# Optimization experiments

Measured on AMD Instinct MI355X. Metric: run time of the kernel, lower is better.

The kernel has to match this reference:

```python
import jax, jax.numpy as jnp
import numpy as np

H = 512          # hidden_size
B, S, L = 32, 2048, 2
D = 2 * H        # encoder output / hidden feature dim


def setup_inputs() -> dict:
    key = jax.random.key(0)
    ks = jax.random.split(key, 9)
    lim1 = 1.0 / np.sqrt(D)
    limv = 1.0 / np.sqrt(H)
    return {
        "hidden": jax.random.normal(ks[0], (L, B, D), jnp.float32),
        "encoder_outputs": jax.random.normal(ks[1], (B, S, D), jnp.float32),
        "mask": jax.random.randint(ks[2], (B, S), 0, 2, jnp.int32),
        "W1_w": jax.random.uniform(ks[3], (H, D), jnp.float32, -lim1, lim1),
        "W1_b": jax.random.uniform(ks[4], (H,), jnp.float32, -lim1, lim1),
        "W2_w": jax.random.uniform(ks[5], (H, D), jnp.float32, -lim1, lim1),
        "W2_b": jax.random.uniform(ks[6], (H,), jnp.float32, -lim1, lim1),
        "V_w": jax.random.uniform(ks[7], (1, H), jnp.float32, -limv, limv),
        "V_b": jax.random.uniform(ks[8], (1,), jnp.float32, -limv, limv),
    }


def reference(hidden, encoder_outputs, mask, W1_w, W1_b, W2_w, W2_b, V_w, V_b):
    # query: last layer hidden state, broadcast over sequence -> [B, 1, D]
    query = hidden[-1][:, None, :]
    # W1(enc) + W2(query): [B, S, H]
    proj = (jnp.einsum('bsd,hd->bsh', encoder_outputs, W1_w) + W1_b
            + jnp.einsum('bqd,hd->bqh', query, W2_w) + W2_b)
    # V projection -> scores [B, S]
    score = jnp.einsum('bsh,h->bs', jnp.tanh(proj), V_w[0]) + V_b[0]
    score = jnp.where(mask == 0, jnp.float32(-1e9), score)
    attn_weights = jax.nn.softmax(score, axis=1)          # [B, S]
    context = jnp.einsum('bs,bsd->bd', attn_weights, encoder_outputs)  # [B, D]
    return context, attn_weights
```

## Files before the change

### kernel.cpp

```cpp
#include <hip/hip_runtime.h>
#include <hip/hip_bf16.h>

#define B_ 32
#define S_ 2048
#define D_ 1024
#define H_ 512
#define M_ (B_*S_)
#define BM 128
#define BN 128
#define BK 64
#define TILE (BM*BK)

typedef __attribute__((ext_vector_type(8))) short short8;
typedef __attribute__((ext_vector_type(4))) float f32x4;

__device__ __forceinline__ unsigned short f2bf(float f){
  return __builtin_bit_cast(unsigned short, __float2bfloat16(f));
}

__device__ __forceinline__ float fast_tanh(float x){
  return 1.f - 2.f*__builtin_amdgcn_rcpf(__expf(2.f*x) + 1.f);
}

__device__ __forceinline__ int swz(int row, int kshort){
  return row*BK + ((kshort & 56) ^ ((row&7)<<3)) + (kshort & 7);
}

__global__ __launch_bounds__(256) void convw_kernel(
    const float* __restrict__ W1, unsigned short* __restrict__ W1s){
  int tid = blockIdx.x*256 + threadIdx.x;
  int n = tid*8;
  int h = n >> 10;
  int k = n & 1023;
  int bn = h >> 7, row = h & 127;
  int kt = k >> 6, kk = k & 63;
  float4 lo = *(const float4*)(W1 + n);
  float4 hi = *(const float4*)(W1 + n + 4);
  short8 r;
  r[0]=(short)f2bf(lo.x); r[1]=(short)f2bf(lo.y); r[2]=(short)f2bf(lo.z); r[3]=(short)f2bf(lo.w);
  r[4]=(short)f2bf(hi.x); r[5]=(short)f2bf(hi.y); r[6]=(short)f2bf(hi.z); r[7]=(short)f2bf(hi.w);
  *(short8*)&W1s[(bn*16 + kt)*TILE + swz(row, kk)] = r;
}

__global__ __launch_bounds__(256) void qbias_kernel(
    const float* __restrict__ hidden, const float* __restrict__ W2,
    const float* __restrict__ W1b, const float* __restrict__ W2b,
    float* __restrict__ qb){
  int b = blockIdx.x, h0 = blockIdx.y*64;
  int wave = threadIdx.x>>6, lane = threadIdx.x&63;
  const float* q = hidden + (size_t)(B_ + b)*D_;
  for (int i=0;i<16;i++){
    int h = h0 + wave*16 + i;
    const float* w = W2 + (size_t)h*D_;
    float s = 0.f;
    #pragma unroll
    for (int it=0; it<4; ++it){
      int d = it*256 + lane*4;
      const float4 qq = *(const float4*)(q+d);
      const float4 ww = *(const float4*)(w+d);
      s += qq.x*ww.x + qq.y*ww.y + qq.z*ww.z + qq.w*ww.w;
    }
    #pragma unroll
    for (int off=1; off<64; off<<=1) s += __shfl_xor(s, off);
    if (lane==0) qb[b*H_ + h] = s + W1b[h] + W2b[h];
  }
}

__global__ __launch_bounds__(256, 3) void score_gemm(
    const float* __restrict__ enc, const unsigned short* __restrict__ W1s,
    const float* __restrict__ qb, const float* __restrict__ Vw,
    float* __restrict__ score_p){
  const int id  = blockIdx.x;
  const int xcd = id & 7;
  const int j   = id >> 3;
  const int bm  = xcd*64 + (j >> 2);
  const int bn  = j & 3;
  const int m0 = bm*BM, h0 = bn*BN;
  const int tid = threadIdx.x, lane = tid&63, wave = tid>>6;
  const int wm = (wave>>1)*64, wn = (wave&1)*64;

  __shared__ __align__(16) unsigned short As[TILE];
  __shared__ __align__(16) unsigned short Bs[2][TILE];

  f32x4 acc[4][4];
  #pragma unroll
  for (int i=0;i<4;i++)
    #pragma unroll
    for (int j2=0;j2<4;j2++)
      acc[i][j2] = (f32x4)(0.f);

  float4 aLo[4], aHi[4];

#define LOAD_A(KT) do{ const int kkx=(KT)*BK; \
  _Pragma("unroll") for (int i=0;i<4;i++){ \
    int c=tid+i*256; int row=c>>3, kc=(c&7)*8; \
    const float4* pa=(const float4*)(enc+(size_t)(m0+row)*D_+kkx+kc); \
    aLo[i]=pa[0]; aHi[i]=pa[1]; } }while(0)

#define GLD_B(KT,P) do{ const unsigned short* bsrc=W1s+(size_t)(bn*16+(KT))*TILE; \
  _Pragma("unroll") for (int i=0;i<4;i++){ \
    __builtin_amdgcn_global_load_lds( \
      (const __attribute__((address_space(1))) unsigned int*)(bsrc+i*2048+tid*8), \
      (__attribute__((address_space(3))) unsigned int*)&Bs[P][i*2048+tid*8], 16,0,0); } }while(0)

#define CVT_A() do{ \
  _Pragma("unroll") for (int i=0;i<4;i++){ \
    int c=tid+i*256; int row=c>>3, kc=(c&7)*8; short8 av; \
    av[0]=(short)f2bf(aLo[i].x); av[1]=(short)f2bf(aLo[i].y); \
    av[2]=(short)f2bf(aLo[i].z); av[3]=(short)f2bf(aLo[i].w); \
    av[4]=(short)f2bf(aHi[i].x); av[5]=(short)f2bf(aHi[i].y); \
    av[6]=(short)f2bf(aHi[i].z); av[7]=(short)f2bf(aHi[i].w); \
    *(short8*)&As[swz(row,kc)] = av; } }while(0)

#define COMPUTE(P) do{ \
  _Pragma("unroll") for (int kh=0; kh<2; ++kh){ \
    const int kb = kh*32 + (lane>>4)*8; \
    short8 af[4], bf[4]; \
    _Pragma("unroll") for (int mi=0;mi<4;mi++){ \
      int row=wm+mi*16+(lane&15); af[mi]=*(const short8*)&As[swz(row,kb)]; } \
    _Pragma("unroll") for (int ni=0;ni<4;ni++){ \
      int row=wn+ni*16+(lane&15); bf[ni]=*(const short8*)&Bs[P][swz(row,kb)]; } \
    _Pragma("unroll") for (int mi=0;mi<4;mi++) \
      _Pragma("unroll") for (int ni=0;ni<4;ni++) \
        acc[mi][ni]=__builtin_amdgcn_mfma_f32_16x16x32_bf16(af[mi],bf[ni],acc[mi][ni],0,0,0); \
  } }while(0)

  LOAD_A(0);
  GLD_B(0,0);
  CVT_A();
  LOAD_A(1);
  GLD_B(1,1);
  asm volatile("s_waitcnt vmcnt(12) lgkmcnt(0)" ::: "memory");
  __builtin_amdgcn_s_barrier();

  #pragma unroll 2
  for (int kt=0; kt<14; ++kt){
    const int p = kt&1;
    COMPUTE(p);
    __builtin_amdgcn_s_barrier();
    GLD_B(kt+2, p);
    CVT_A();
    LOAD_A(kt+2);
    asm volatile("s_waitcnt lgkmcnt(0)" ::: "memory");
    __builtin_amdgcn_s_barrier();
  }
  COMPUTE(0);
  __builtin_amdgcn_s_barrier();
  CVT_A();
  asm volatile("s_waitcnt lgkmcnt(0)" ::: "memory");
  __builtin_amdgcn_s_barrier();
  COMPUTE(1);

  const int bidx = m0 >> 11;
  float qv[4], vwv[4];
  #pragma unroll
  for (int ni=0;ni<4;ni++){
    int h = h0 + wn + ni*16 + (lane&15);
    qv[ni]  = qb[bidx*H_ + h];
    vwv[ni] = Vw[h];
  }
  __shared__ float psum[4][BM];
  #pragma unroll
  for (int mi=0;mi<4;mi++){
    #pragma unroll
    for (int r=0;r<4;r++){
      float s = 0.f;
      #pragma unroll
      for (int ni=0;ni<4;ni++) s += fast_tanh(acc[mi][ni][r] + qv[ni]) * vwv[ni];
      s += __shfl_xor(s,1); s += __shfl_xor(s,2);
      s += __shfl_xor(s,4); s += __shfl_xor(s,8);
      if ((lane&15)==0){
        int m = wm + mi*16 + ((lane>>4)<<2) + r;
        psum[wave][m] = s;
      }
    }
  }
  __syncthreads();
  if (tid < BM){
    int w0 = (tid>>6)*2;
    score_p[(size_t)bn*M_ + m0 + tid] = psum[w0][tid] + psum[w0+1][tid];
  }
}

__global__ __launch_bounds__(256) void softmax_kernel(
    const float* __restrict__ score_p, const int* __restrict__ mask,
    float* __restrict__ attn){
  int b = blockIdx.x, tid = threadIdx.x;
  int wave = tid>>6, lane = tid&63;
  __shared__ float red[8];
  float v[8];
  float mx = -1e30f;
  #pragma unroll
  for (int i=0;i<8;i++){
    int idx = b*S_ + tid + i*256;
    float sc = score_p[idx] + score_p[M_+idx] + score_p[2*M_+idx] + score_p[3*M_+idx];
    v[i] = (mask[idx]==0) ? -1e9f : sc;
    mx = fmaxf(mx, v[i]);
  }
  #pragma unroll
  for (int off=1; off<64; off<<=1) mx = fmaxf(mx, __shfl_xor(mx, off));
  if (lane==0) red[wave] = mx;
  __syncthreads();
  mx = fmaxf(fmaxf(red[0],red[1]), fmaxf(red[2],red[3]));
  float sum = 0.f;
  #pragma unroll
  for (int i=0;i<8;i++){ v[i] = __expf(v[i]-mx); sum += v[i]; }
  #pragma unroll
  for (int off=1; off<64; off<<=1) sum += __shfl_xor(sum, off);
  if (lane==0) red[4+wave] = sum;
  __syncthreads();
  float inv = 1.f/(red[4]+red[5]+red[6]+red[7]);
  #pragma unroll
  for (int i=0;i<8;i++) attn[b*S_ + tid + i*256] = v[i]*inv;
}

__global__ __launch_bounds__(256) void context_kernel(
    const float* __restrict__ enc, const float* __restrict__ attn,
    float* __restrict__ ctx){
  int b = blockIdx.x, sc = blockIdx.y;
  int s0 = sc*64;
  int d4 = threadIdx.x*4;
  const float* ep = enc + ((size_t)b*S_ + s0)*D_ + d4;
  const float* ap = attn + b*S_ + s0;
  float4 a0 = make_float4(0.f,0.f,0.f,0.f);
  float4 a1 = make_float4(0.f,0.f,0.f,0.f);
  #pragma unroll 4
  for (int i=0;i<64;i+=2){
    float w0 = ap[i], w1 = ap[i+1];
    float4 e0 = *(const float4*)(ep + (size_t)i*D_);
    float4 e1 = *(const float4*)(ep + (size_t)(i+1)*D_);
    a0.x = fmaf(w0, e0.x, a0.x); a0.y = fmaf(w0, e0.y, a0.y);
    a0.z = fmaf(w0, e0.z, a0.z); a0.w = fmaf(w0, e0.w, a0.w);
    a1.x = fmaf(w1, e1.x, a1.x); a1.y = fmaf(w1, e1.y, a1.y);
    a1.z = fmaf(w1, e1.z, a1.z); a1.w = fmaf(w1, e1.w, a1.w);
  }
  float* o = ctx + b*D_ + d4;
  atomicAdd(o+0, a0.x+a1.x); atomicAdd(o+1, a0.y+a1.y);
  atomicAdd(o+2, a0.z+a1.z); atomicAdd(o+3, a0.w+a1.w);
}

extern "C" void kernel_launch(void* const* d_in, const int* in_sizes, int n_in,
                              void* d_out, int out_size, void* d_ws, size_t ws_size,
                              hipStream_t stream){
  const float* hidden = (const float*)d_in[0];
  const float* enc    = (const float*)d_in[1];
  const int*   mask   = (const int*)d_in[2];
  const float* W1w    = (const float*)d_in[3];
  const float* W1b    = (const float*)d_in[4];
  const float* W2w    = (const float*)d_in[5];
  const float* W2b    = (const float*)d_in[6];
  const float* Vw     = (const float*)d_in[7];
  float* out = (float*)d_out;

  float* qb           = (float*)d_ws;
  float* score_p      = qb + B_*H_;
  unsigned short* W1s = (unsigned short*)(score_p + 4*M_);

  hipMemsetAsync(out, 0, (size_t)B_*D_*sizeof(float), stream);

  convw_kernel  <<<H_*D_/8/256,     256, 0, stream>>>(W1w, W1s);
  qbias_kernel  <<<dim3(B_, H_/64), 256, 0, stream>>>(hidden, W2w, W1b, W2b, qb);
  score_gemm    <<<4*(M_/BM),       256, 0, stream>>>(enc, W1s, qb, Vw, score_p);
  softmax_kernel<<<B_,              256, 0, stream>>>(score_p, mask, out + B_*D_);
  context_kernel<<<dim3(B_, 32),    256, 0, stream>>>(enc, out + B_*D_, out);
}
```

Measured before the change: 187.3 us.

## Load W1 fragments directly into registers in MFMA order, double-buffer A in LDS

The weight conversion kernel now writes W1 in a per-lane MFMA fragment order, so the GEMM can load B operands straight from global memory into registers (register double-buffered) instead of staging them through LDS. LDS is repurposed as a double buffer for the converted A tile, which removes one barrier per k-step. The cost is higher register pressure (occupancy hint lowered from 3 to 2) and B being fetched per wave from global/L2 rather than shared across the block.

```diff
diff --git a/kernel.cpp b/kernel.cpp
--- a/kernel.cpp
+++ b/kernel.cpp
@@ -27,19 +27,19 @@
 }
 
 __global__ __launch_bounds__(256) void convw_kernel(
-    const float* __restrict__ W1, unsigned short* __restrict__ W1s){
-  int tid = blockIdx.x*256 + threadIdx.x;
-  int n = tid*8;
-  int h = n >> 10;
-  int k = n & 1023;
-  int bn = h >> 7, row = h & 127;
-  int kt = k >> 6, kk = k & 63;
-  float4 lo = *(const float4*)(W1 + n);
-  float4 hi = *(const float4*)(W1 + n + 4);
-  short8 r;
-  r[0]=(short)f2bf(lo.x); r[1]=(short)f2bf(lo.y); r[2]=(short)f2bf(lo.z); r[3]=(short)f2bf(lo.w);
-  r[4]=(short)f2bf(hi.x); r[5]=(short)f2bf(hi.y); r[6]=(short)f2bf(hi.z); r[7]=(short)f2bf(hi.w);
-  *(short8*)&W1s[(bn*16 + kt)*TILE + swz(row, kk)] = r;
+    const float* __restrict__ W1, unsigned short* __restrict__ W1f){
+  int g = blockIdx.x*256 + threadIdx.x;
+  int lane = g & 63, r = g >> 6;
+  int kh = r & 1, ni = (r>>1)&3, wh = (r>>3)&1, kt = (r>>4)&15, bn = r>>8;
+  int h  = bn*128 + wh*64 + ni*16 + (lane&15);
+  int k0 = kt*64 + kh*32 + (lane>>4)*8;
+  const float* src = W1 + (size_t)h*D_ + k0;
+  float4 lo = *(const float4*)src;
+  float4 hi = *(const float4*)(src+4);
+  short8 v;
+  v[0]=(short)f2bf(lo.x); v[1]=(short)f2bf(lo.y); v[2]=(short)f2bf(lo.z); v[3]=(short)f2bf(lo.w);
+  v[4]=(short)f2bf(hi.x); v[5]=(short)f2bf(hi.y); v[6]=(short)f2bf(hi.z); v[7]=(short)f2bf(hi.w);
+  *(short8*)&W1f[(size_t)g*8] = v;
 }
 
 __global__ __launch_bounds__(256) void qbias_kernel(
@@ -66,8 +66,8 @@
   }
 }
 
-__global__ __launch_bounds__(256, 3) void score_gemm(
-    const float* __restrict__ enc, const unsigned short* __restrict__ W1s,
+__global__ __launch_bounds__(256, 2) void score_gemm(
+    const float* __restrict__ enc, const unsigned short* __restrict__ W1f,
     const float* __restrict__ qb, const float* __restrict__ Vw,
     float* __restrict__ score_p){
   const int id  = blockIdx.x;
@@ -77,10 +77,9 @@
   const int bn  = j & 3;
   const int m0 = bm*BM, h0 = bn*BN;
   const int tid = threadIdx.x, lane = tid&63, wave = tid>>6;
-  const int wm = (wave>>1)*64, wn = (wave&1)*64;
-
-  __shared__ __align__(16) unsigned short As[TILE];
-  __shared__ __align__(16) unsigned short Bs[2][TILE];
+  const int wm = (wave>>1)*64, wh = wave&1, wn = wh*64;
+
+  __shared__ __align__(16) unsigned short As[2][TILE];
 
   f32x4 acc[4][4];
   #pragma unroll
@@ -90,6 +89,7 @@
       acc[i][j2] = (f32x4)(0.f);
 
   float4 aLo[4], aHi[4];
+  short8 b0[4][2], b1[4][2];
 
 #define LOAD_A(KT) do{ const int kkx=(KT)*BK; \
   _Pragma("unroll") for (int i=0;i<4;i++){ \
@@ -97,59 +97,59 @@
     const float4* pa=(const float4*)(enc+(size_t)(m0+row)*D_+kkx+kc); \
     aLo[i]=pa[0]; aHi[i]=pa[1]; } }while(0)
 
-#define GLD_B(KT,P) do{ const unsigned short* bsrc=W1s+(size_t)(bn*16+(KT))*TILE; \
-  _Pragma("unroll") for (int i=0;i<4;i++){ \
-    __builtin_amdgcn_global_load_lds( \
-      (const __attribute__((address_space(1))) unsigned int*)(bsrc+i*2048+tid*8), \
-      (__attribute__((address_space(3))) unsigned int*)&Bs[P][i*2048+tid*8], 16,0,0); } }while(0)
-
-#define CVT_A() do{ \
+#define CVT_A(P) do{ \
   _Pragma("unroll") for (int i=0;i<4;i++){ \
     int c=tid+i*256; int row=c>>3, kc=(c&7)*8; short8 av; \
     av[0]=(short)f2bf(aLo[i].x); av[1]=(short)f2bf(aLo[i].y); \
     av[2]=(short)f2bf(aLo[i].z); av[3]=(short)f2bf(aLo[i].w); \
     av[4]=(short)f2bf(aHi[i].x); av[5]=(short)f2bf(aHi[i].y); \
     av[6]=(short)f2bf(aHi[i].z); av[7]=(short)f2bf(aHi[i].w); \
-    *(short8*)&As[swz(row,kc)] = av; } }while(0)
-
-#define COMPUTE(P) do{ \
+    *(short8*)&As[P][swz(row,kc)] = av; } }while(0)
+
+#define GLOB_B(KT, BB) do{ \
+  const size_t sb = (size_t)(((bn*16+(KT))*2+wh)*8)*512 + lane*8; \
+  _Pragma("unroll") for (int ni=0;ni<4;ni++) \
+    _Pragma("unroll") for (int kh=0;kh<2;kh++) \
+      BB[ni][kh] = *(const short8*)&W1f[sb + (size_t)(ni*2+kh)*512]; }while(0)
+
+#define COMPUTE(P, BB) do{ \
   _Pragma("unroll") for (int kh=0; kh<2; ++kh){ \
     const int kb = kh*32 + (lane>>4)*8; \
-    short8 af[4], bf[4]; \
+    short8 af[4]; \
     _Pragma("unroll") for (int mi=0;mi<4;mi++){ \
-      int row=wm+mi*16+(lane&15); af[mi]=*(const short8*)&As[swz(row,kb)]; } \
-    _Pragma("unroll") for (int ni=0;ni<4;ni++){ \
-      int row=wn+ni*16+(lane&15); bf[ni]=*(const short8*)&Bs[P][swz(row,kb)]; } \
+      int row=wm+mi*16+(lane&15); af[mi]=*(const short8*)&As[P][swz(row,kb)]; } \
     _Pragma("unroll") for (int mi=0;mi<4;mi++) \
       _Pragma("unroll") for (int ni=0;ni<4;ni++) \
-        acc[mi][ni]=__builtin_amdgcn_mfma_f32_16x16x32_bf16(af[mi],bf[ni],acc[mi][ni],0,0,0); \
+        acc[mi][ni]=__builtin_amdgcn_mfma_f32_16x16x32_bf16(af[mi],BB[ni][kh],acc[mi][ni],0,0,0); \
   } }while(0)
 
+#define BODY(KT, BC, BN_) do{ \
+  GLOB_B((KT)+1, BN_); \
+  __builtin_amdgcn_sched_barrier(0); \
+  COMPUTE((KT)&1, BC); \
+  CVT_A(((KT)+1)&1); \
+  LOAD_A((KT)+2); \
+  asm volatile("s_waitcnt lgkmcnt(0)" ::: "memory"); \
+  __builtin_amdgcn_s_barrier(); }while(0)
+
   LOAD_A(0);
-  GLD_B(0,0);
-  CVT_A();
+  GLOB_B(0, b0);
+  CVT_A(0);
   LOAD_A(1);
-  GLD_B(1,1);
-  asm volatile("s_waitcnt vmcnt(12) lgkmcnt(0)" ::: "memory");
-  __builtin_amdgcn_s_barrier();
-
-  #pragma unroll 2
-  for (int kt=0; kt<14; ++kt){
-    const int p = kt&1;
-    COMPUTE(p);
-    __builtin_amdgcn_s_barrier();
-    GLD_B(kt+2, p);
-    CVT_A();
-    LOAD_A(kt+2);
-    asm volatile("s_waitcnt lgkmcnt(0)" ::: "memory");
-    __builtin_amdgcn_s_barrier();
-  }
-  COMPUTE(0);
-  __builtin_amdgcn_s_barrier();
-  CVT_A();
   asm volatile("s_waitcnt lgkmcnt(0)" ::: "memory");
   __builtin_amdgcn_s_barrier();
-  COMPUTE(1);
+
+  for (int k2=0; k2<7; ++k2){
+    BODY(2*k2,   b0, b1);
+    BODY(2*k2+1, b1, b0);
+  }
+  GLOB_B(15, b1);
+  __builtin_amdgcn_sched_barrier(0);
+  COMPUTE(0, b0);
+  CVT_A(1);
+  asm volatile("s_waitcnt lgkmcnt(0)" ::: "memory");
+  __builtin_amdgcn_s_barrier();
+  COMPUTE(1, b1);
 
   const int bidx = m0 >> 11;
   float qv[4], vwv[4];
@@ -254,13 +254,13 @@
 
   float* qb           = (float*)d_ws;
   float* score_p      = qb + B_*H_;
-  unsigned short* W1s = (unsigned short*)(score_p + 4*M_);
+  unsigned short* W1f = (unsigned short*)(score_p + 4*M_);
 
   hipMemsetAsync(out, 0, (size_t)B_*D_*sizeof(float), stream);
 
-  convw_kernel  <<<H_*D_/8/256,     256, 0, stream>>>(W1w, W1s);
+  convw_kernel  <<<H_*D_/8/256,     256, 0, stream>>>(W1w, W1f);
   qbias_kernel  <<<dim3(B_, H_/64), 256, 0, stream>>>(hidden, W2w, W1b, W2b, qb);
-  score_gemm    <<<4*(M_/BM),       256, 0, stream>>>(enc, W1s, qb, Vw, score_p);
+  score_gemm    <<<4*(M_/BM),       256, 0, stream>>>(enc, W1f, qb, Vw, score_p);
   softmax_kernel<<<B_,              256, 0, stream>>>(score_p, mask, out + B_*D_);
   context_kernel<<<dim3(B_, 32),    256, 0, stream>>>(enc, out + B_*D_, out);
 }
```

After: 192.8 us. 1.03x slower.

## Widen score GEMM N-tile to 256 and replace context atomics with two-pass reduce

Applied to the files above, without the earlier changes.

The score GEMM N-tile doubles from 128 to 256 columns. Each block now covers half of H, so the fp32 encoder tile is loaded and converted to bf16 only twice instead of four times, and only two partial score planes are written. This costs a larger LDS footprint and twice the accumulators, with launch bounds dropped to two blocks per CU. Separately, the atomicAdd-based context accumulation and the output memset are replaced by partial-sum writes plus a small reduce kernel, adding one launch.

```diff
diff --git a/kernel.cpp b/kernel.cpp
--- a/kernel.cpp
+++ b/kernel.cpp
@@ -7,9 +7,10 @@
 #define H_ 512
 #define M_ (B_*S_)
 #define BM 128
-#define BN 128
+#define BN 256
 #define BK 64
-#define TILE (BM*BK)
+#define TILE_A (BM*BK)
+#define TILE_B (BN*BK)
 
 typedef __attribute__((ext_vector_type(8))) short short8;
 typedef __attribute__((ext_vector_type(4))) float f32x4;
@@ -28,18 +29,17 @@
 
 __global__ __launch_bounds__(256) void convw_kernel(
     const float* __restrict__ W1, unsigned short* __restrict__ W1s){
-  int tid = blockIdx.x*256 + threadIdx.x;
-  int n = tid*8;
-  int h = n >> 10;
-  int k = n & 1023;
-  int bn = h >> 7, row = h & 127;
+  int g = blockIdx.x*256 + threadIdx.x;
+  int n = g*8;
+  int h = n >> 10, k = n & 1023;
+  int bn = h >> 8, row = h & 255;
   int kt = k >> 6, kk = k & 63;
   float4 lo = *(const float4*)(W1 + n);
   float4 hi = *(const float4*)(W1 + n + 4);
   short8 r;
   r[0]=(short)f2bf(lo.x); r[1]=(short)f2bf(lo.y); r[2]=(short)f2bf(lo.z); r[3]=(short)f2bf(lo.w);
   r[4]=(short)f2bf(hi.x); r[5]=(short)f2bf(hi.y); r[6]=(short)f2bf(hi.z); r[7]=(short)f2bf(hi.w);
-  *(short8*)&W1s[(bn*16 + kt)*TILE + swz(row, kk)] = r;
+  *(short8*)&W1s[(size_t)(bn*16 + kt)*TILE_B + swz(row, kk)] = r;
 }
 
 __global__ __launch_bounds__(256) void qbias_kernel(
@@ -66,27 +66,30 @@
   }
 }
 
-__global__ __launch_bounds__(256, 3) void score_gemm(
+__global__ __launch_bounds__(256, 2) void score_gemm(
     const float* __restrict__ enc, const unsigned short* __restrict__ W1s,
     const float* __restrict__ qb, const float* __restrict__ Vw,
     float* __restrict__ score_p){
   const int id  = blockIdx.x;
   const int xcd = id & 7;
   const int j   = id >> 3;
-  const int bm  = xcd*64 + (j >> 2);
-  const int bn  = j & 3;
+  const int bm  = xcd*64 + (j >> 1);
+  const int bn  = j & 1;
   const int m0 = bm*BM, h0 = bn*BN;
   const int tid = threadIdx.x, lane = tid&63, wave = tid>>6;
-  const int wm = (wave>>1)*64, wn = (wave&1)*64;
-
-  __shared__ __align__(16) unsigned short As[TILE];
-  __shared__ __align__(16) unsigned short Bs[2][TILE];
-
-  f32x4 acc[4][4];
+  const int wm = (wave>>1)*64, wn = (wave&1)*128;
+
+  __shared__ __align__(16) unsigned short lds[TILE_A + 2*TILE_B];
+  unsigned short* As = lds;
+  unsigned short* Bs0 = lds + TILE_A;
+  unsigned short* Bs1 = lds + TILE_A + TILE_B;
+  float* psum = (float*)lds;
+
+  f32x4 acc[4][8];
   #pragma unroll
   for (int i=0;i<4;i++)
     #pragma unroll
-    for (int j2=0;j2<4;j2++)
+    for (int j2=0;j2<8;j2++)
       acc[i][j2] = (f32x4)(0.f);
 
   float4 aLo[4], aHi[4];
@@ -97,11 +100,11 @@
     const float4* pa=(const float4*)(enc+(size_t)(m0+row)*D_+kkx+kc); \
     aLo[i]=pa[0]; aHi[i]=pa[1]; } }while(0)
 
-#define GLD_B(KT,P) do{ const unsigned short* bsrc=W1s+(size_t)(bn*16+(KT))*TILE; \
-  _Pragma("unroll") for (int i=0;i<4;i++){ \
+#define GLD_B(KT,BP) do{ const unsigned short* bsrc=W1s+(size_t)(bn*16+(KT))*TILE_B; \
+  _Pragma("unroll") for (int i=0;i<8;i++){ \
     __builtin_amdgcn_global_load_lds( \
       (const __attribute__((address_space(1))) unsigned int*)(bsrc+i*2048+tid*8), \
-      (__attribute__((address_space(3))) unsigned int*)&Bs[P][i*2048+tid*8], 16,0,0); } }while(0)
+      (__attribute__((address_space(3))) unsigned int*)&(BP)[i*2048+tid*8], 16,0,0); } }while(0)
 
 #define CVT_A() do{ \
   _Pragma("unroll") for (int i=0;i<4;i++){ \
@@ -112,73 +115,72 @@
     av[6]=(short)f2bf(aHi[i].z); av[7]=(short)f2bf(aHi[i].w); \
     *(short8*)&As[swz(row,kc)] = av; } }while(0)
 
-#define COMPUTE(P) do{ \
+#define COMPUTE(BP) do{ \
   _Pragma("unroll") for (int kh=0; kh<2; ++kh){ \
     const int kb = kh*32 + (lane>>4)*8; \
-    short8 af[4], bf[4]; \
+    short8 af[4]; \
     _Pragma("unroll") for (int mi=0;mi<4;mi++){ \
       int row=wm+mi*16+(lane&15); af[mi]=*(const short8*)&As[swz(row,kb)]; } \
-    _Pragma("unroll") for (int ni=0;ni<4;ni++){ \
-      int row=wn+ni*16+(lane&15); bf[ni]=*(const short8*)&Bs[P][swz(row,kb)]; } \
-    _Pragma("unroll") for (int mi=0;mi<4;mi++) \
-      _Pragma("unroll") for (int ni=0;ni<4;ni++) \
-        acc[mi][ni]=__builtin_amdgcn_mfma_f32_16x16x32_bf16(af[mi],bf[ni],acc[mi][ni],0,0,0); \
+    _Pragma("unroll") for (int ni=0;ni<8;ni++){ \
+      int row=wn+ni*16+(lane&15); \
+      short8 bf=*(const short8*)&(BP)[swz(row,kb)]; \
+      _Pragma("unroll") for (int mi=0;mi<4;mi++) \
+        acc[mi][ni]=__builtin_amdgcn_mfma_f32_16x16x32_bf16(af[mi],bf,acc[mi][ni],0,0,0); \
+    } \
   } }while(0)
 
   LOAD_A(0);
-  GLD_B(0,0);
+  GLD_B(0, Bs0);
   CVT_A();
   LOAD_A(1);
-  GLD_B(1,1);
-  asm volatile("s_waitcnt vmcnt(12) lgkmcnt(0)" ::: "memory");
-  __builtin_amdgcn_s_barrier();
-
-  #pragma unroll 2
+  GLD_B(1, Bs1);
+  asm volatile("s_waitcnt vmcnt(16) lgkmcnt(0)" ::: "memory");
+  __builtin_amdgcn_s_barrier();
+
   for (int kt=0; kt<14; ++kt){
-    const int p = kt&1;
-    COMPUTE(p);
+    if (kt&1) COMPUTE(Bs1); else COMPUTE(Bs0);
     __builtin_amdgcn_s_barrier();
-    GLD_B(kt+2, p);
+    if (kt&1) GLD_B(kt+2, Bs1); else GLD_B(kt+2, Bs0);
     CVT_A();
     LOAD_A(kt+2);
     asm volatile("s_waitcnt lgkmcnt(0)" ::: "memory");
     __builtin_amdgcn_s_barrier();
   }
-  COMPUTE(0);
+  COMPUTE(Bs0);
   __builtin_amdgcn_s_barrier();
   CVT_A();
   asm volatile("s_waitcnt lgkmcnt(0)" ::: "memory");
   __builtin_amdgcn_s_barrier();
-  COMPUTE(1);
+  COMPUTE(Bs1);
 
   const int bidx = m0 >> 11;
-  float qv[4], vwv[4];
-  #pragma unroll
-  for (int ni=0;ni<4;ni++){
+  float qv[8], vwv[8];
+  #pragma unroll
+  for (int ni=0;ni<8;ni++){
     int h = h0 + wn + ni*16 + (lane&15);
     qv[ni]  = qb[bidx*H_ + h];
     vwv[ni] = Vw[h];
   }
-  __shared__ float psum[4][BM];
+  __builtin_amdgcn_s_barrier();
   #pragma unroll
   for (int mi=0;mi<4;mi++){
     #pragma unroll
     for (int r=0;r<4;r++){
       float s = 0.f;
       #pragma unroll
-      for (int ni=0;ni<4;ni++) s += fast_tanh(acc[mi][ni][r] + qv[ni]) * vwv[ni];
+      for (int ni=0;ni<8;ni++) s += fast_tanh(acc[mi][ni][r] + qv[ni]) * vwv[ni];
       s += __shfl_xor(s,1); s += __shfl_xor(s,2);
       s += __shfl_xor(s,4); s += __shfl_xor(s,8);
       if ((lane&15)==0){
         int m = wm + mi*16 + ((lane>>4)<<2) + r;
-        psum[wave][m] = s;
+        psum[wave*BM + m] = s;
       }
     }
   }
   __syncthreads();
   if (tid < BM){
     int w0 = (tid>>6)*2;
-    score_p[(size_t)bn*M_ + m0 + tid] = psum[w0][tid] + psum[w0+1][tid];
+    score_p[(size_t)bn*M_ + m0 + tid] = psum[w0*BM + tid] + psum[(w0+1)*BM + tid];
   }
 }
 
@@ -193,7 +195,7 @@
   #pragma unroll
   for (int i=0;i<8;i++){
     int idx = b*S_ + tid + i*256;
-    float sc = score_p[idx] + score_p[M_+idx] + score_p[2*M_+idx] + score_p[3*M_+idx];
+    float sc = score_p[idx] + score_p[M_+idx];
     v[i] = (mask[idx]==0) ? -1e9f : sc;
     mx = fmaxf(mx, v[i]);
   }
@@ -214,9 +216,9 @@
   for (int i=0;i<8;i++) attn[b*S_ + tid + i*256] = v[i]*inv;
 }
 
-__global__ __launch_bounds__(256) void context_kernel(
+__global__ __launch_bounds__(256) void context_part(
     const float* __restrict__ enc, const float* __restrict__ attn,
-    float* __restrict__ ctx){
+    float* __restrict__ ctx_p){
   int b = blockIdx.x, sc = blockIdx.y;
   int s0 = sc*64;
   int d4 = threadIdx.x*4;
@@ -234,9 +236,19 @@
     a1.x = fmaf(w1, e1.x, a1.x); a1.y = fmaf(w1, e1.y, a1.y);
     a1.z = fmaf(w1, e1.z, a1.z); a1.w = fmaf(w1, e1.w, a1.w);
   }
-  float* o = ctx + b*D_ + d4;
-  atomicAdd(o+0, a0.x+a1.x); atomicAdd(o+1, a0.y+a1.y);
-  atomicAdd(o+2, a0.z+a1.z); atomicAdd(o+3, a0.w+a1.w);
+  float4 t = make_float4(a0.x+a1.x, a0.y+a1.y, a0.z+a1.z, a0.w+a1.w);
+  *(float4*)(ctx_p + ((size_t)b*32 + sc)*D_ + d4) = t;
+}
+
+__global__ __launch_bounds__(256) void context_reduce(
+    const float* __restrict__ ctx_p, float* __restrict__ ctx){
+  int b = blockIdx.x;
+  int d4 = threadIdx.x*4;
+  f32x4 s = (f32x4)(0.f);
+  #pragma unroll 8
+  for (int sc=0; sc<32; ++sc)
+    s += *(const f32x4*)(ctx_p + ((size_t)b*32 + sc)*D_ + d4);
+  *(f32x4*)(ctx + (size_t)b*D_ + d4) = s;
 }
 
 extern "C" void kernel_launch(void* const* d_in, const int* in_sizes, int n_in,
@@ -254,13 +266,13 @@
 
   float* qb           = (float*)d_ws;
   float* score_p      = qb + B_*H_;
-  unsigned short* W1s = (unsigned short*)(score_p + 4*M_);
-
-  hipMemsetAsync(out, 0, (size_t)B_*D_*sizeof(float), stream);
+  unsigned short* W1s = (unsigned short*)(score_p + 2*M_);
+  float* ctx_p        = (float*)(W1s + H_*D_);
 
   convw_kernel  <<<H_*D_/8/256,     256, 0, stream>>>(W1w, W1s);
   qbias_kernel  <<<dim3(B_, H_/64), 256, 0, stream>>>(hidden, W2w, W1b, W2b, qb);
-  score_gemm    <<<4*(M_/BM),       256, 0, stream>>>(enc, W1s, qb, Vw, score_p);
+  score_gemm    <<<2*(M_/BM),       256, 0, stream>>>(enc, W1s, qb, Vw, score_p);
   softmax_kernel<<<B_,              256, 0, stream>>>(score_p, mask, out + B_*D_);
-  context_kernel<<<dim3(B_, 32),    256, 0, stream>>>(enc, out + B_*D_, out);
-}
+  context_part  <<<dim3(B_, 32),    256, 0, stream>>>(enc, out + B_*D_, ctx_p);
+  context_reduce<<<B_,              256, 0, stream>>>(ctx_p, out);
+}
```

Measured after the change: 672.6 us. +259.1%, slower.
